# Kernel tuning notes

Hardware: AMD Instinct MI355X
Metric: run time of the kernel (lower is better)

## Reference

```python
import jax, jax.numpy as jnp
import numpy as np
import math

B, T_FUT, T_LOOK, D, H = 8, 512, 2048, 1024, 16
HD = D // H


def setup_inputs() -> dict:
    key = jax.random.key(0)
    ks = jax.random.split(key, 12)
    xav = 1.0 / math.sqrt(D)  # approx xavier_uniform scale for square [D,D]
    return {
        "encoded_representation": jax.random.normal(ks[0], (B, T_LOOK, D), jnp.float32),
        "future_queries": jax.random.normal(ks[1], (B, T_FUT, D), jnp.float32),
        "decoder_lengths": jax.random.randint(ks[2], (B,), 1, T_FUT + 1),
        "encoder_lengths": jax.random.randint(ks[3], (B,), 1, T_LOOK + 1),
        "wq_w": jax.random.normal(ks[4], (D, D), jnp.float32) * xav,
        "wq_b": jnp.zeros((D,), jnp.float32),
        "wk_w": jax.random.normal(ks[5], (D, D), jnp.float32) * xav,
        "wk_b": jnp.zeros((D,), jnp.float32),
        "wv_w": jax.random.normal(ks[6], (D, D), jnp.float32) * xav,
        "wv_b": jnp.zeros((D,), jnp.float32),
        "wo_w": jax.random.normal(ks[7], (D, D), jnp.float32) * xav,
        "wo_b": jnp.zeros((D,), jnp.float32),
    }


def reference(encoded_representation, future_queries, decoder_lengths, encoder_lengths,
              wq_w, wq_b, wk_w, wk_b, wv_w, wv_b, wo_w, wo_b):
    # variable-length padding mask: [B, 1, T_fut, T_look]
    dec_valid = jnp.arange(T_FUT)[None, :] < decoder_lengths[:, None]   # [B, T_fut]
    enc_valid = jnp.arange(T_LOOK)[None, :] < encoder_lengths[:, None]  # [B, T_look]
    mask = dec_valid[:, None, :, None] & enc_valid[:, None, None, :]

    # torch nn.Linear: y = x @ W^T + b
    Q = (future_queries @ wq_w.T + wq_b).reshape(B, T_FUT, H, HD)
    K = (encoded_representation @ wk_w.T + wk_b).reshape(B, T_LOOK, H, HD)
    V = (encoded_representation @ wv_w.T + wv_b).reshape(B, T_LOOK, H, HD)

    scores = jnp.einsum("bqhd,bkhd->bhqk", Q, K) / math.sqrt(HD)
    # NOTE: faithful to source, which fills masked positions with -1e-09 (not -1e9)
    scores = jnp.where(mask, scores, jnp.float32(-1e-09))
    probs = jax.nn.softmax(scores, axis=-1)

    attended = jnp.einsum("bhqk,bkhd->bqhd", probs, V).reshape(B, T_FUT, D)
    return attended @ wo_w.T + wo_b
```

## Files before the change

### kernel.cpp

```cpp
#include <hip/hip_runtime.h>

typedef __attribute__((ext_vector_type(4))) float f32x4;
typedef __attribute__((ext_vector_type(8))) short s16x8;

__device__ __forceinline__ ushort f2bf(float f) {
  unsigned u = __float_as_uint(f);
  return (ushort)((u + 0x7fffu + ((u >> 16) & 1u)) >> 16);
}

__global__ __launch_bounds__(256) void cvt_bf16(const float4* __restrict__ in,
                                                ushort* __restrict__ out, int n4) {
  int stride = gridDim.x * blockDim.x;
  for (int i = blockIdx.x * blockDim.x + threadIdx.x; i < n4; i += stride) {
    float4 v = in[i];
    uint2 o;
    o.x = (unsigned)f2bf(v.x) | ((unsigned)f2bf(v.y) << 16);
    o.y = (unsigned)f2bf(v.z) | ((unsigned)f2bf(v.w) << 16);
    *(uint2*)(out + (size_t)i * 4) = o;
  }
}

__global__ __launch_bounds__(256) void cvt_bf16_w4(const float4* __restrict__ a,
                                                   const float4* __restrict__ b,
                                                   const float4* __restrict__ c,
                                                   const float4* __restrict__ d,
                                                   ushort* __restrict__ oa, ushort* __restrict__ ob,
                                                   ushort* __restrict__ oc, ushort* __restrict__ od) {
  int idx = blockIdx.x * 256 + threadIdx.x;
  int sel = idx >> 18, k = idx & 262143;
  const float4* src = sel == 0 ? a : sel == 1 ? b : sel == 2 ? c : d;
  ushort* dst = sel == 0 ? oa : sel == 1 ? ob : sel == 2 ? oc : od;
  float4 v = src[k];
  uint2 o;
  o.x = (unsigned)f2bf(v.x) | ((unsigned)f2bf(v.y) << 16);
  o.y = (unsigned)f2bf(v.z) | ((unsigned)f2bf(v.w) << 16);
  *(uint2*)(dst + (size_t)k * 4) = o;
}

__device__ __forceinline__ void gload_lds16(const void* g, void* l) {
  __builtin_amdgcn_global_load_lds((const __attribute__((address_space(1))) void*)g,
                                   (__attribute__((address_space(3))) void*)l, 16, 0, 0);
}

__global__ __launch_bounds__(512, 1) void gemm256_fused(
    const ushort* __restrict__ enc16, const ushort* __restrict__ fq16,
    const ushort* __restrict__ Bkv, const ushort* __restrict__ Bq,
    const float* __restrict__ wk_b, const float* __restrict__ wv_b,
    const float* __restrict__ wq_b,
    ushort* __restrict__ Ko, ushort* __restrict__ Vt, ushort* __restrict__ Qo,
    float* __restrict__ Tsum, const int* __restrict__ dlen,
    const int* __restrict__ elen, float qscale) {
  __shared__ char lds[131072];
  const int tid = threadIdx.x;
  const int lane = tid & 63, wid = tid >> 6;
  const int g = lane >> 4, r = lane & 15;
  const int wm = wid >> 2, wn = wid & 3;
  const int bid = blockIdx.x;

  const ushort* Amat;
  const ushort* Bmat;
  int m0, n0, role;
  if (bid < 512) {
    const int xcd = bid & 7, inner = bid >> 3;
    const int i = inner & 7;
    m0 = (i * 8 + ((xcd + i) & 7)) * 256;
    n0 = (inner >> 3) * 256;
    Amat = enc16;
    Bmat = Bkv;
    if (n0 < 1024) {
      role = 0;
      if ((m0 & 2047) >= elen[m0 >> 11]) return;
    } else {
      role = 1;
    }
  } else {
    const int q = bid - 512;
    m0 = (q & 15) * 256;
    n0 = (q >> 4) * 256;
    Amat = fq16;
    Bmat = Bq;
    role = 2;
    if ((m0 & 511) >= dlen[m0 >> 9]) return;
  }
  const size_t rowb = 2048;

  const int srow = tid >> 3;
  const int scb = (((tid & 7) ^ (srow & 7)) << 4);
  const char* Asrc = (const char*)Amat + (size_t)(m0 + srow) * rowb + scb;
  const char* Bsrc = (const char*)Bmat + (size_t)(n0 + srow) * rowb + scb;

  auto sAh = [&](int kt, int h) {
    char* d0 = lds + (kt & 1) * 32768 + h * 16384 + tid * 16;
    const char* s0 = Asrc + (size_t)(h * 128) * rowb + (size_t)kt * 128;
    gload_lds16(s0, d0);
    gload_lds16(s0 + (size_t)64 * rowb, d0 + 8192);
  };
  auto sBh = [&](int kt, int h) {
    char* d0 = lds + 65536 + (kt & 1) * 32768 + h * 16384 + tid * 16;
    const char* s0 = Bsrc + (size_t)(h * 128) * rowb + (size_t)kt * 128;
    gload_lds16(s0, d0);
    gload_lds16(s0 + (size_t)64 * rowb, d0 + 8192);
  };

  const int cb0 = (g * 16) ^ ((r & 7) << 4);
  const int cb1 = (64 + g * 16) ^ ((r & 7) << 4);

  f32x4 acc[8][4] = {};

  sAh(0, 0); sAh(0, 1); sBh(0, 0); sBh(0, 1); sBh(1, 0); sBh(1, 1);
  asm volatile("s_waitcnt vmcnt(4)" ::: "memory");
  __builtin_amdgcn_s_barrier();

#define MFMA_(a, b, c) __builtin_amdgcn_mfma_f32_16x16x32_bf16(a, b, c, 0, 0, 0)
#define PH(AB, Q, STAGE, WAIT)                                                 \
  {                                                                            \
    s16x8 aq0 = *(const s16x8*)(AB + (2 * (Q)) * 2048 + cb0);                  \
    s16x8 aq1 = *(const s16x8*)(AB + (2 * (Q)) * 2048 + cb1);                  \
    s16x8 aq2 = *(const s16x8*)(AB + (2 * (Q) + 1) * 2048 + cb0);              \
    s16x8 aq3 = *(const s16x8*)(AB + (2 * (Q) + 1) * 2048 + cb1);              \
    STAGE;                                                                     \
    __builtin_amdgcn_s_barrier();                                              \
    asm volatile("s_waitcnt lgkmcnt(0)" ::: "memory");                         \
    __builtin_amdgcn_sched_barrier(0);                                         \
    __builtin_amdgcn_s_setprio(1);                                             \
    _Pragma("unroll") for (int ni = 0; ni < 4; ++ni)                           \
        acc[2 * (Q)][ni] = MFMA_(aq0, bfr[ni][0], acc[2 * (Q)][ni]);           \
    _Pragma("unroll") for (int ni = 0; ni < 4; ++ni)                           \
        acc[2 * (Q) + 1][ni] = MFMA_(aq2, bfr[ni][0], acc[2 * (Q) + 1][ni]);   \
    _Pragma("unroll") for (int ni = 0; ni < 4; ++ni)                           \
        acc[2 * (Q)][ni] = MFMA_(aq1, bfr[ni][1], acc[2 * (Q)][ni]);           \
    _Pragma("unroll") for (int ni = 0; ni < 4; ++ni)                           \
        acc[2 * (Q) + 1][ni] = MFMA_(aq3, bfr[ni][1], acc[2 * (Q) + 1][ni]);   \
    __builtin_amdgcn_s_setprio(0);                                             \
    WAIT;                                                                      \
    __builtin_amdgcn_s_barrier();                                              \
  }
#define LOADB(BB)                                                              \
  _Pragma("unroll") for (int ni = 0; ni < 4; ++ni) {                           \
    bfr[ni][0] = *(const s16x8*)(BB + ni * 2048 + cb0);                        \
    bfr[ni][1] = *(const s16x8*)(BB + ni * 2048 + cb1);                        \
  }

  const int NIT = 8;
  const char* AbB = lds + wm * 16384 + r * 128;
  const char* BbB = lds + 65536 + (wn >> 1) * 16384 + (wn & 1) * 8192 + r * 128;

  for (int it = 0; it < NIT; ++it) {
    const bool st = (it + 1 < NIT);
    const int k1 = 2 * it + 1, k2 = 2 * it + 2, k3 = 2 * it + 3;
    s16x8 bfr[4][2];
    LOADB(BbB);
    PH(AbB, 0, sAh(k1, 0), );
    PH(AbB, 1, sAh(k1, 1), );
    PH(AbB, 2, if (st) sBh(k2, 0), );
    PH(AbB, 3, if (st) sBh(k2, 1),
       if (st) { asm volatile("s_waitcnt vmcnt(4)" ::: "memory"); } else {
         asm volatile("s_waitcnt vmcnt(0)" ::: "memory");
       });
    const char* Ab1 = AbB + 32768;
    const char* Bb1 = BbB + 32768;
    LOADB(Bb1);
    PH(Ab1, 0, if (st) sAh(k2, 0), );
    PH(Ab1, 1, if (st) sAh(k2, 1), );
    PH(Ab1, 2, if (st) sBh(k3, 0), );
    PH(Ab1, 3, if (st) sBh(k3, 1),
       if (st) { asm volatile("s_waitcnt vmcnt(4)" ::: "memory"); });
  }
#undef PH
#undef LOADB
#undef MFMA_

  if (role != 1) {
    ushort* C = (role == 2) ? Qo : Ko;
    const float* bias0 = (role == 2) ? wq_b : wk_b;
    const float sc = (role == 2) ? qscale : 1.0f;
#pragma unroll
    for (int ni = 0; ni < 4; ++ni) {
      const int col = wn * 64 + ni * 16 + r;
      const float bv = bias0[n0 + col];
#pragma unroll
      for (int i = 0; i < 8; ++i)
#pragma unroll
        for (int j = 0; j < 4; ++j) {
          const int row = wm * 128 + i * 16 + g * 4 + j;
          *(ushort*)(lds + ((row * 512 + col * 2) ^ (((row >> 2) & 7) << 4))) =
              f2bf((acc[i][ni][j] + bv) * sc);
        }
    }
    __syncthreads();
    const int c = tid & 31, r0 = tid >> 5;
#pragma unroll
    for (int u = 0; u < 16; ++u) {
      const int row = u * 16 + r0;
      s16x8 v = *(const s16x8*)(lds + ((row * 512 + c * 16) ^ (((row >> 2) & 7) << 4)));
      *(s16x8*)(C + (size_t)(m0 + row) * 1024 + n0 + c * 8) = v;
    }
  } else {
    const int nv0 = n0 - 1024;
    const int bb = m0 >> 11, tt0 = m0 & 2047;
#pragma unroll
    for (int ni = 0; ni < 4; ++ni) {
      const int nv = nv0 + wn * 64 + ni * 16 + r;
      const float bv = wv_b[nv];
#pragma unroll
      for (int qq = 0; qq < 2; ++qq) {
        float s = 0.0f;
#pragma unroll
        for (int ii = 0; ii < 4; ++ii)
#pragma unroll
          for (int j = 0; j < 4; ++j) s += acc[qq * 4 + ii][ni][j];
        s += __shfl_xor(s, 16);
        s += __shfl_xor(s, 32);
        if (g == 0) {
          const int gt = (m0 + (wm * 2 + qq) * 64) >> 6;
          Tsum[((size_t)((gt >> 5) * 16 + (nv >> 6)) * 33 + (gt & 31)) * 64 + (nv & 63)] =
              s + 64.0f * bv;
        }
      }
    }
#pragma unroll
    for (int ni = 0; ni < 4; ++ni) {
      const int rowl = wn * 64 + ni * 16 + r;
      const float bv = wv_b[nv0 + rowl];
#pragma unroll
      for (int i = 0; i < 8; ++i)
#pragma unroll
        for (int j = 0; j < 4; ++j) {
          const int coll = wm * 128 + i * 16 + g * 4 + j;
          *(ushort*)(lds + ((rowl * 512 + coll * 2) ^ ((rowl & 7) << 4))) =
              f2bf(acc[i][ni][j] + bv);
        }
    }
    __syncthreads();
    const int c = tid & 31, r0 = tid >> 5;
#pragma unroll
    for (int u = 0; u < 16; ++u) {
      const int row = u * 16 + r0;
      s16x8 v = *(const s16x8*)(lds + ((row * 512 + c * 16) ^ ((row & 7) << 4)));
      *(s16x8*)(Vt + ((size_t)bb * 1024 + nv0 + row) * 2048 + tt0 + c * 8) = v;
    }
  }
}

template <int EPI>
__global__ __launch_bounds__(256) void gemm_bt(const ushort* __restrict__ A,
                                               const ushort* __restrict__ B,
                                               const float* __restrict__ bias,
                                               void* __restrict__ Cout, float oscale,
                                               int M, int N, int K) {
  __shared__ ushort As[128 * 32];
  __shared__ ushort Bs[128 * 32];
  const int tid = threadIdx.x;
  const int lane = tid & 63, w = tid >> 6;
  const int g = lane >> 4, r = lane & 15;
  const int m0 = blockIdx.x * 128, n0 = blockIdx.y * 128;
  const int wm = (w >> 1) * 64, wn = (w & 1) * 64;

  const int srow = tid >> 2;
  const int scb = (tid & 3) * 16;
  const char* Ag = (const char*)(A + (size_t)(m0 + srow) * K) + scb;
  const char* Bg = (const char*)(B + (size_t)(n0 + srow) * K) + scb;
  char* AsB = (char*)As + (tid & 192) * 16;
  char* BsB = (char*)Bs + (tid & 192) * 16;
  const size_t rowskip = (size_t)64 * K * sizeof(ushort);

  f32x4 acc[4][4] = {};

  for (int k0 = 0; k0 < K; k0 += 32) {
    gload_lds16(Ag + (size_t)k0 * 2, AsB);
    gload_lds16(Ag + rowskip + (size_t)k0 * 2, AsB + 4096);
    gload_lds16(Bg + (size_t)k0 * 2, BsB);
    gload_lds16(Bg + rowskip + (size_t)k0 * 2, BsB + 4096);
    __syncthreads();
    s16x8 af[4], bf[4];
#pragma unroll
    for (int i = 0; i < 4; ++i) af[i] = *(const s16x8*)&As[(wm + i * 16 + r) * 32 + g * 8];
#pragma unroll
    for (int i = 0; i < 4; ++i) bf[i] = *(const s16x8*)&Bs[(wn + i * 16 + r) * 32 + g * 8];
#pragma unroll
    for (int mi = 0; mi < 4; ++mi)
#pragma unroll
      for (int ni = 0; ni < 4; ++ni)
        acc[mi][ni] =
            __builtin_amdgcn_mfma_f32_16x16x32_bf16(af[mi], bf[ni], acc[mi][ni], 0, 0, 0);
    __syncthreads();
  }

  if constexpr (EPI == 0) {
    ushort* C = (ushort*)Cout;
#pragma unroll
    for (int ni = 0; ni < 4; ++ni) {
      const int n = n0 + wn + ni * 16 + r;
      const float bv = bias[n];
#pragma unroll
      for (int mi = 0; mi < 4; ++mi) {
        const int mb = m0 + wm + mi * 16 + g * 4;
#pragma unroll
        for (int j = 0; j < 4; ++j)
          C[(size_t)(mb + j) * N + n] = f2bf((acc[mi][ni][j] + bv) * oscale);
      }
    }
  } else {
    float* C = (float*)Cout;
#pragma unroll
    for (int ni = 0; ni < 4; ++ni) {
      const int n = n0 + wn + ni * 16 + r;
      const float bv = bias[n];
#pragma unroll
      for (int mi = 0; mi < 4; ++mi) {
        const int mb = m0 + wm + mi * 16 + g * 4;
#pragma unroll
        for (int j = 0; j < 4; ++j)
          C[(size_t)(mb + j) * N + n] = acc[mi][ni][j] + bv;
      }
    }
  }
}

__global__ __launch_bounds__(64) void vsuffix(float* __restrict__ T) {
  const int bh = blockIdx.x;
  const int d = threadIdx.x;
  float* p = T + (size_t)bh * 33 * 64 + d;
  float run = 0.0f;
  p[32 * 64] = 0.0f;
  for (int t = 31; t >= 0; --t) {
    run += p[t * 64];
    p[t * 64] = run;
  }
}

__device__ __forceinline__ ushort* swz(ushort* base, int row, int colb) {
  return (ushort*)((char*)base + row * 128 + (colb ^ ((row & 7) << 4)));
}

__global__ __launch_bounds__(256) void attn_fwd(
    const ushort* __restrict__ Q, const ushort* __restrict__ Km,
    const ushort* __restrict__ Vt, const float* __restrict__ Vsuf,
    const int* __restrict__ dlen, const int* __restrict__ elen,
    ushort* __restrict__ Oatt) {
  const int tid = threadIdx.x;
  const int lane = tid & 63, w = tid >> 6;
  const int g = lane >> 4, r = lane & 15;
  const int qt = blockIdx.x, b = blockIdx.y, h = blockIdx.z;
  const int dl = dlen[b], el = elen[b];
  const float* VS = Vsuf + (size_t)(b * 16 + h) * 33 * 64;

  if (qt * 64 >= dl) {
    const int qrow = qt * 64 + w * 16 + g * 4;
#pragma unroll
    for (int dt = 0; dt < 4; ++dt) {
      const ushort hv = f2bf(VS[dt * 16 + r] * (1.0f / 2048.0f));
#pragma unroll
      for (int j = 0; j < 4; ++j)
        Oatt[(size_t)(b * 512 + qrow + j) * 1024 + h * 64 + dt * 16 + r] = hv;
    }
    return;
  }

  __shared__ ushort Ks[64 * 64];
  __shared__ ushort Vs[64 * 64];
  __shared__ ushort Ps[4 * 16 * 64];
  ushort* PsW = Ps + w * 16 * 64;
  const int qbase = qt * 64 + w * 16;

  s16x8 qf[2];
  {
    const ushort* qp = Q + (size_t)(b * 512 + qbase + r) * 1024 + h * 64 + g * 8;
    qf[0] = *(const s16x8*)qp;
    qf[1] = *(const s16x8*)(qp + 32);
  }

  f32x4 o[4] = {};
  float lrow[4] = {0.0f, 0.0f, 0.0f, 0.0f};
  bool qok[4];
#pragma unroll
  for (int j = 0; j < 4; ++j) qok[j] = (qbase + g * 4 + j) < dl;

  const int sr = tid >> 3;
  const int sc8 = (tid & 7) * 8;
  const int scb = sc8 * 2;
  const ushort* Kg = Km + (size_t)(b * 2048 + sr) * 1024 + h * 64 + sc8;
  const ushort* Vg = Vt + ((size_t)b * 1024 + h * 64 + sr) * 2048 + sc8;

  const int t_last = (el - 1) >> 6;

  s16x8 pk0, pk1, pv0, pv1;
  {
    pk0 = *(const s16x8*)(Kg);
    pk1 = *(const s16x8*)(Kg + (size_t)32 * 1024);
    pv0 = *(const s16x8*)(Vg);
    pv1 = *(const s16x8*)(Vg + (size_t)32 * 2048);
  }

  for (int t = 0; t <= t_last; ++t) {
    *(s16x8*)swz(Ks, sr, scb) = pk0;
    *(s16x8*)swz(Ks, sr + 32, scb) = pk1;
    *(s16x8*)swz(Vs, sr, scb) = pv0;
    *(s16x8*)swz(Vs, sr + 32, scb) = pv1;
    __syncthreads();

    if (t < t_last) {
      const int kv0 = (t + 1) * 64;
      pk0 = *(const s16x8*)(Kg + (size_t)kv0 * 1024);
      pk1 = *(const s16x8*)(Kg + (size_t)(kv0 + 32) * 1024);
      pv0 = *(const s16x8*)(Vg + kv0);
      pv1 = *(const s16x8*)(Vg + (size_t)32 * 2048 + kv0);
    }

    const int kv0 = t * 64;
    float p[4][4];
#pragma unroll
    for (int nt = 0; nt < 4; ++nt) {
      f32x4 s = {};
      s16x8 kf0 = *(const s16x8*)swz(Ks, nt * 16 + r, g * 16);
      s16x8 kf1 = *(const s16x8*)swz(Ks, nt * 16 + r, 64 + g * 16);
      s = __builtin_amdgcn_mfma_f32_16x16x32_bf16(qf[0], kf0, s, 0, 0, 0);
      s = __builtin_amdgcn_mfma_f32_16x16x32_bf16(qf[1], kf1, s, 0, 0, 0);
      const bool kok = (kv0 + nt * 16 + r) < el;
#pragma unroll
      for (int j = 0; j < 4; ++j) {
        const float pe = __builtin_amdgcn_exp2f(s[j]);
        p[nt][j] = (kok && qok[j]) ? pe : 1.0f;
      }
    }
#pragma unroll
    for (int nt = 0; nt < 4; ++nt)
#pragma unroll
      for (int j = 0; j < 4; ++j) lrow[j] += p[nt][j];

#pragma unroll
    for (int nt = 0; nt < 4; ++nt) {
#pragma unroll
      for (int jp = 0; jp < 4; jp += 2) {
        unsigned pk;
        asm("v_cvt_pk_bf16_f32 %0, %1, %2" : "=v"(pk) : "v"(p[nt][jp]), "v"(p[nt][jp + 1]));
        *swz(PsW, g * 4 + jp, (nt * 16 + r) * 2) = (ushort)pk;
        *swz(PsW, g * 4 + jp + 1, (nt * 16 + r) * 2) = (ushort)(pk >> 16);
      }
    }

#pragma unroll
    for (int kc = 0; kc < 2; ++kc) {
      s16x8 pf = *(const s16x8*)swz(PsW, r, kc * 64 + g * 16);
#pragma unroll
      for (int dt = 0; dt < 4; ++dt) {
        s16x8 vf = *(const s16x8*)swz(Vs, dt * 16 + r, kc * 64 + g * 16);
        o[dt] = __builtin_amdgcn_mfma_f32_16x16x32_bf16(pf, vf, o[dt], 0, 0, 0);
      }
    }
    __syncthreads();
  }

  const float tailcnt = (float)(2048 - (t_last + 1) * 64);
  const float* VT = VS + (t_last + 1) * 64;
#pragma unroll
  for (int dt = 0; dt < 4; ++dt) {
    const float tv = VT[dt * 16 + r];
#pragma unroll
    for (int j = 0; j < 4; ++j) o[dt][j] += tv;
  }

  float inv[4];
#pragma unroll
  for (int j = 0; j < 4; ++j) {
    float s = lrow[j];
    s += __shfl_xor(s, 1);
    s += __shfl_xor(s, 2);
    s += __shfl_xor(s, 4);
    s += __shfl_xor(s, 8);
    inv[j] = 1.0f / (s + tailcnt);
  }
#pragma unroll
  for (int dt = 0; dt < 4; ++dt)
#pragma unroll
    for (int j = 0; j < 4; ++j)
      Oatt[(size_t)(b * 512 + qbase + g * 4 + j) * 1024 + h * 64 + dt * 16 + r] =
          f2bf(o[dt][j] * inv[j]);
}

extern "C" void kernel_launch(void* const* d_in, const int* in_sizes, int n_in,
                              void* d_out, int out_size, void* d_ws, size_t ws_size,
                              hipStream_t stream) {
  const float* enc  = (const float*)d_in[0];
  const float* fq   = (const float*)d_in[1];
  const int* dlen   = (const int*)d_in[2];
  const int* elen   = (const int*)d_in[3];
  const float* wq_w = (const float*)d_in[4];
  const float* wq_b = (const float*)d_in[5];
  const float* wk_w = (const float*)d_in[6];
  const float* wk_b = (const float*)d_in[7];
  const float* wv_w = (const float*)d_in[8];
  const float* wv_b = (const float*)d_in[9];
  const float* wo_w = (const float*)d_in[10];
  const float* wo_b = (const float*)d_in[11];

  char* ws = (char*)d_ws;
  ushort* enc16 = (ushort*)(ws + 0);
  ushort* fq16  = (ushort*)(ws + 33554432);
  float*  Vsuf  = (float*)(ws + 41943040 + 2097152 * 4);
  ushort* wq16  = (ushort*)(ws + 41943040);
  ushort* wk16  = (ushort*)(ws + 44040192);
  ushort* wv16  = (ushort*)(ws + 46137344);
  ushort* wo16  = (ushort*)(ws + 48234496);
  ushort* Qw    = (ushort*)(ws + 52428800);
  ushort* Kw    = (ushort*)(ws + 60817408);
  ushort* Vtw   = (ushort*)(ws + 94371840);
  ushort* attw  = (ushort*)(ws + 127926272);

  cvt_bf16<<<2048, 256, 0, stream>>>((const float4*)enc, enc16, 16384 * 1024 / 4);
  cvt_bf16<<<1024, 256, 0, stream>>>((const float4*)fq, fq16, 4096 * 1024 / 4);
  cvt_bf16_w4<<<4096, 256, 0, stream>>>((const float4*)wq_w, (const float4*)wk_w,
                                        (const float4*)wv_w, (const float4*)wo_w,
                                        wq16, wk16, wv16, wo16);

  const float qscale = 0.125f * 1.44269504088896340736f;
  gemm256_fused<<<576, 512, 0, stream>>>(enc16, fq16, wk16, wq16, wk_b, wv_b, wq_b,
                                         Kw, Vtw, Qw, Vsuf, dlen, elen, qscale);
  vsuffix<<<128, 64, 0, stream>>>(Vsuf);

  attn_fwd<<<dim3(8, 8, 16), 256, 0, stream>>>(Qw, Kw, Vtw, Vsuf, dlen, elen, attw);

  gemm_bt<2><<<dim3(32, 8), 256, 0, stream>>>(attw, wo16, wo_b, d_out, 1.0f, 4096, 1024, 1024);
}
```

Measured before the change: 203.0 us.

## Compute V tile sums via encoder row-sum GEMM and skip masked V tiles

Per-64-row V column sums are no longer taken from the V projection epilogue. They now come from summing encoder rows in 64-row groups (encsum) and projecting those sums through Wv with a small GEMM. This lets the fused projection kernel skip V tiles beyond each batch's encoder length, not only K tiles, which cuts GEMM work. The cost is two extra small launches, and the tile sums are now computed from bf16-rounded encoder sums, which changes numerics slightly. The attention output buffer is also moved to alias the fq16 region.

Result: slower. 224.9 us (+10.8%).

```diff
diff --git a/kernel.cpp b/kernel.cpp
--- a/kernel.cpp
+++ b/kernel.cpp
@@ -6,6 +6,9 @@
 __device__ __forceinline__ ushort f2bf(float f) {
   unsigned u = __float_as_uint(f);
   return (ushort)((u + 0x7fffu + ((u >> 16) & 1u)) >> 16);
+}
+__device__ __forceinline__ float bf2f(ushort u) {
+  return __uint_as_float((unsigned)u << 16);
 }
 
 __global__ __launch_bounds__(256) void cvt_bf16(const float4* __restrict__ in,
@@ -37,6 +40,25 @@
   *(uint2*)(dst + (size_t)k * 4) = o;
 }
 
+__global__ __launch_bounds__(256) void encsum(const ushort* __restrict__ enc16,
+                                              ushort* __restrict__ S) {
+  const int blk = blockIdx.x;
+  const int tid = threadIdx.x;
+  const ushort* p = enc16 + (size_t)blk * 64 * 1024 + tid * 4;
+  float a0 = 0, a1 = 0, a2 = 0, a3 = 0;
+  for (int row = 0; row < 64; ++row) {
+    ushort4 v = *(const ushort4*)(p + (size_t)row * 1024);
+    a0 += bf2f(v.x);
+    a1 += bf2f(v.y);
+    a2 += bf2f(v.z);
+    a3 += bf2f(v.w);
+  }
+  uint2 o;
+  o.x = (unsigned)f2bf(a0) | ((unsigned)f2bf(a1) << 16);
+  o.y = (unsigned)f2bf(a2) | ((unsigned)f2bf(a3) << 16);
+  *(uint2*)(S + (size_t)blk * 1024 + tid * 4) = o;
+}
+
 __device__ __forceinline__ void gload_lds16(const void* g, void* l) {
   __builtin_amdgcn_global_load_lds((const __attribute__((address_space(1))) void*)g,
                                    (__attribute__((address_space(3))) void*)l, 16, 0, 0);
@@ -48,8 +70,7 @@
     const float* __restrict__ wk_b, const float* __restrict__ wv_b,
     const float* __restrict__ wq_b,
     ushort* __restrict__ Ko, ushort* __restrict__ Vt, ushort* __restrict__ Qo,
-    float* __restrict__ Tsum, const int* __restrict__ dlen,
-    const int* __restrict__ elen, float qscale) {
+    const int* __restrict__ dlen, const int* __restrict__ elen, float qscale) {
   __shared__ char lds[131072];
   const int tid = threadIdx.x;
   const int lane = tid & 63, wid = tid >> 6;
@@ -67,12 +88,8 @@
     n0 = (inner >> 3) * 256;
     Amat = enc16;
     Bmat = Bkv;
-    if (n0 < 1024) {
-      role = 0;
-      if ((m0 & 2047) >= elen[m0 >> 11]) return;
-    } else {
-      role = 1;
-    }
+    if ((m0 & 2047) >= elen[m0 >> 11]) return;
+    role = (n0 < 1024) ? 0 : 1;
   } else {
     const int q = bid - 512;
     m0 = (q & 15) * 256;
@@ -200,26 +217,6 @@
     const int bb = m0 >> 11, tt0 = m0 & 2047;
 #pragma unroll
     for (int ni = 0; ni < 4; ++ni) {
-      const int nv = nv0 + wn * 64 + ni * 16 + r;
-      const float bv = wv_b[nv];
-#pragma unroll
-      for (int qq = 0; qq < 2; ++qq) {
-        float s = 0.0f;
-#pragma unroll
-        for (int ii = 0; ii < 4; ++ii)
-#pragma unroll
-          for (int j = 0; j < 4; ++j) s += acc[qq * 4 + ii][ni][j];
-        s += __shfl_xor(s, 16);
-        s += __shfl_xor(s, 32);
-        if (g == 0) {
-          const int gt = (m0 + (wm * 2 + qq) * 64) >> 6;
-          Tsum[((size_t)((gt >> 5) * 16 + (nv >> 6)) * 33 + (gt & 31)) * 64 + (nv & 63)] =
-              s + 64.0f * bv;
-        }
-      }
-    }
-#pragma unroll
-    for (int ni = 0; ni < 4; ++ni) {
       const int rowl = wn * 64 + ni * 16 + r;
       const float bv = wv_b[nv0 + rowl];
 #pragma unroll
@@ -286,8 +283,8 @@
     __syncthreads();
   }
 
-  if constexpr (EPI == 0) {
-    ushort* C = (ushort*)Cout;
+  if constexpr (EPI == 2) {
+    float* C = (float*)Cout;
 #pragma unroll
     for (int ni = 0; ni < 4; ++ni) {
       const int n = n0 + wn + ni * 16 + r;
@@ -297,21 +294,24 @@
         const int mb = m0 + wm + mi * 16 + g * 4;
 #pragma unroll
         for (int j = 0; j < 4; ++j)
-          C[(size_t)(mb + j) * N + n] = f2bf((acc[mi][ni][j] + bv) * oscale);
+          C[(size_t)(mb + j) * N + n] = acc[mi][ni][j] + bv;
       }
     }
   } else {
-    float* C = (float*)Cout;
+    float* T = (float*)Cout;
 #pragma unroll
     for (int ni = 0; ni < 4; ++ni) {
       const int n = n0 + wn + ni * 16 + r;
-      const float bv = bias[n];
+      const float bv = 64.0f * bias[n];
 #pragma unroll
       for (int mi = 0; mi < 4; ++mi) {
         const int mb = m0 + wm + mi * 16 + g * 4;
 #pragma unroll
-        for (int j = 0; j < 4; ++j)
-          C[(size_t)(mb + j) * N + n] = acc[mi][ni][j] + bv;
+        for (int j = 0; j < 4; ++j) {
+          const int row = mb + j;
+          T[((size_t)((row >> 5) * 16 + (n >> 6)) * 33 + (row & 31)) * 64 + (n & 63)] =
+              acc[mi][ni][j] + bv;
+        }
       }
     }
   }
@@ -497,15 +497,16 @@
   char* ws = (char*)d_ws;
   ushort* enc16 = (ushort*)(ws + 0);
   ushort* fq16  = (ushort*)(ws + 33554432);
-  float*  Vsuf  = (float*)(ws + 41943040 + 2097152 * 4);
+  ushort* attw  = (ushort*)(ws + 33554432);
   ushort* wq16  = (ushort*)(ws + 41943040);
   ushort* wk16  = (ushort*)(ws + 44040192);
   ushort* wv16  = (ushort*)(ws + 46137344);
   ushort* wo16  = (ushort*)(ws + 48234496);
+  ushort* Sb16  = (ushort*)(ws + 50331648);
+  float*  Vsuf  = (float*)(ws + 50855936);
   ushort* Qw    = (ushort*)(ws + 52428800);
   ushort* Kw    = (ushort*)(ws + 60817408);
   ushort* Vtw   = (ushort*)(ws + 94371840);
-  ushort* attw  = (ushort*)(ws + 127926272);
 
   cvt_bf16<<<2048, 256, 0, stream>>>((const float4*)enc, enc16, 16384 * 1024 / 4);
   cvt_bf16<<<1024, 256, 0, stream>>>((const float4*)fq, fq16, 4096 * 1024 / 4);
@@ -513,9 +514,12 @@
                                         (const float4*)wv_w, (const float4*)wo_w,
                                         wq16, wk16, wv16, wo16);
 
+  encsum<<<256, 256, 0, stream>>>(enc16, Sb16);
+  gemm_bt<3><<<dim3(2, 8), 256, 0, stream>>>(Sb16, wv16, wv_b, Vsuf, 1.0f, 256, 1024, 1024);
+
   const float qscale = 0.125f * 1.44269504088896340736f;
   gemm256_fused<<<576, 512, 0, stream>>>(enc16, fq16, wk16, wq16, wk_b, wv_b, wq_b,
-                                         Kw, Vtw, Qw, Vsuf, dlen, elen, qscale);
+                                         Kw, Vtw, Qw, dlen, elen, qscale);
   vsuffix<<<128, 64, 0, stream>>>(Vsuf);
 
   attn_fwd<<<dim3(8, 8, 16), 256, 0, stream>>>(Qw, Kw, Vtw, Vsuf, dlen, elen, attw);
```
